# Kernel optimization log

Measured on AMD Instinct MI355X. Metric: run time of the kernel, lower is better.

The kernel has to match this reference:

```python
import jax, jax.numpy as jnp
import numpy as np

B, C, H, W = 16, 64, 128, 128
C8 = C // 8


def setup_inputs() -> dict:
    key = jax.random.key(0)
    ks = jax.random.split(key, 8)
    s = 0.05
    return {
        "x": jax.random.normal(ks[0], (B, C, H, W), dtype=jnp.float32),
        "Wq": jax.random.normal(ks[1], (C8, C), dtype=jnp.float32) * s,
        "bq": jax.random.normal(ks[2], (C8,), dtype=jnp.float32) * s,
        "Wk": jax.random.normal(ks[3], (C8, C), dtype=jnp.float32) * s,
        "bk": jax.random.normal(ks[4], (C8,), dtype=jnp.float32) * s,
        "Wv": jax.random.normal(ks[5], (C, C), dtype=jnp.float32) * s,
        "bv": jax.random.normal(ks[6], (C,), dtype=jnp.float32) * s,
        "gamma": jnp.zeros((1,), dtype=jnp.float32),
    }


def _criss_cross(x, Wq, bq, Wk, bk, Wv, bv, gamma):
    # 1x1 convs == channel-mixing matmuls
    q = jnp.einsum("bchw,oc->bohw", x, Wq) + bq[None, :, None, None]  # [B,C8,H,W]
    k = jnp.einsum("bchw,oc->bohw", x, Wk) + bk[None, :, None, None]  # [B,C8,H,W]
    v = jnp.einsum("bchw,oc->bohw", x, Wv) + bv[None, :, None, None]  # [B,C,H,W]

    h = x.shape[2]
    # column (H-axis) attention scores; diagonal masked to -inf
    energy_H = jnp.einsum("bchw,bciw->bhwi", q, k)  # [B,H,W,H]
    diag = jnp.eye(h, dtype=bool)[None, :, None, :]  # mask where query row == key row
    energy_H = jnp.where(diag, -jnp.inf, energy_H)
    # row (W-axis) attention scores
    energy_W = jnp.einsum("bchw,bchj->bhwj", q, k)  # [B,H,W,W]

    # joint softmax over concatenated H+W axis
    att = jax.nn.softmax(jnp.concatenate([energy_H, energy_W], axis=3), axis=3)
    att_H = att[:, :, :, :h]    # [B,H,W,H]
    att_W = att[:, :, :, h:]    # [B,H,W,W]

    out_H = jnp.einsum("bhwi,bciw->bchw", att_H, v)
    out_W = jnp.einsum("bhwj,bchj->bchw", att_W, v)
    return gamma[0] * (out_H + out_W) + x


def reference(x, Wq, bq, Wk, bk, Wv, bv, gamma):
    return _criss_cross(x, Wq, bq, Wk, bk, Wv, bv, gamma)
```

## Files before the change

### kernel.cpp

```cpp
#include <hip/hip_runtime.h>

#define HW 128
#define CC 64
#define NB 16
#define LOG2E 1.44269504088896f

typedef _Float16 h1;
typedef _Float16 h2 __attribute__((ext_vector_type(2)));
typedef _Float16 half8 __attribute__((ext_vector_type(8)));
typedef float float16v __attribute__((ext_vector_type(16)));
typedef uint uv4 __attribute__((ext_vector_type(4)));

__device__ __forceinline__ uint packh2(float a, float b) {
#if __has_builtin(__builtin_amdgcn_cvt_pkrtz)
  return __builtin_bit_cast(uint, __builtin_amdgcn_cvt_pkrtz(a, b));
#else
  h2 v; v[0] = (h1)a; v[1] = (h1)b; return __builtin_bit_cast(uint, v);
#endif
}
__device__ __forceinline__ ushort f2h(float a) { h1 v = (h1)a; return __builtin_bit_cast(ushort, v); }
__device__ __forceinline__ float  h2f(ushort a) { return (float)__builtin_bit_cast(h1, a); }

__device__ __forceinline__ float fexp2(float x) {
#if __has_builtin(__builtin_amdgcn_exp2f)
  return __builtin_amdgcn_exp2f(x);
#else
  return exp2f(x);
#endif
}

__device__ __forceinline__ float16v mfma16(uv4 a, uv4 b, float16v c) {
  return __builtin_amdgcn_mfma_f32_32x32x16_f16(
      __builtin_bit_cast(half8, a), __builtin_bit_cast(half8, b), c, 0, 0, 0);
}

__global__ __launch_bounds__(256) void k_prep(
    const float* __restrict__ Wq, const float* __restrict__ bq,
    const float* __restrict__ Wk, const float* __restrict__ bk,
    const float* __restrict__ Wv, const float* __restrict__ bv,
    ushort* __restrict__ W_frag, float* __restrict__ bias_f)
{
  int idx = blockIdx.x * 256 + threadIdx.x;
  if (idx < 6144) {
    int g = idx >> 3, e = idx & 7;
    int kshi = g / 96, o = g % 96;
    int ks = kshi >> 1, hi = kshi & 1;
    int c = 8 * hi + 16 * ks + e;
    float val = (o < 8)  ? Wq[o * 64 + c] * LOG2E
              : (o < 16) ? Wk[(o - 8) * 64 + c]
              : (o < 80) ? Wv[(o - 16) * 64 + c] : 0.f;
    W_frag[idx] = f2h(val);
  }
  if (blockIdx.x == 0 && threadIdx.x < 96) {
    int t = threadIdx.x;
    bias_f[t] = (t < 8) ? bq[t] * LOG2E : (t < 16) ? bk[t - 8] : (t < 80) ? bv[t - 16] : 0.f;
  }
}

__global__ __launch_bounds__(256, 4) void k_projW(
    const float* __restrict__ x, const ushort* __restrict__ W_frag,
    const float* __restrict__ bias_f,
    ushort* __restrict__ qT, ushort* __restrict__ kT,
    ushort* __restrict__ v,
    ushort* __restrict__ oW_, float* __restrict__ mW_, float* __restrict__ sW_)
{
  alignas(16) __shared__ uint V_l[64 * 64];
  alignas(16) __shared__ ushort qk_l[128 * 24];
  __shared__ float bias_l[96];

  int t = threadIdx.x;
  int lane = t & 63, wv = t >> 6, hi = lane >> 5;
  int b = blockIdx.x >> 7, r = blockIdx.x & 127;
  if (t < 96) bias_l[t] = bias_f[t];

  int w = 32 * wv + (lane & 31);
  const float* xw = x + (size_t)(b * CC) * (HW * HW) + (size_t)r * HW + w;
  const size_t PL = (size_t)HW * HW;

  float xv[32];
  #pragma unroll
  for (int ks = 0; ks < 4; ++ks) {
    int c0 = 8 * hi + 16 * ks;
    #pragma unroll
    for (int e = 0; e < 8; ++e)
      xv[ks * 8 + e] = xw[(size_t)(c0 + e) * PL];
  }
  __builtin_amdgcn_sched_barrier(0);

  float16v acc0 = {}, acc1 = {}, acc2 = {};
  #pragma unroll
  for (int ks = 0; ks < 4; ++ks) {
    uv4 Bx;
    #pragma unroll
    for (int e2 = 0; e2 < 4; ++e2)
      Bx[e2] = packh2(xv[ks * 8 + 2 * e2], xv[ks * 8 + 2 * e2 + 1]);
    const ushort* wf = W_frag + (size_t)(ks * 2 + hi) * 96 * 8;
    uv4 a0 = *(const uv4*)(wf + (lane & 31) * 8);
    uv4 a1 = *(const uv4*)(wf + ((lane & 31) + 32) * 8);
    uv4 a2 = *(const uv4*)(wf + ((lane & 31) + 64) * 8);
    acc0 = mfma16(a0, Bx, acc0);
    acc1 = mfma16(a1, Bx, acc1);
    acc2 = mfma16(a2, Bx, acc2);
  }
  __syncthreads();

  #pragma unroll
  for (int reg = 0; reg < 16; ++reg) {
    int orow = (reg & 3) + 8 * (reg >> 2) + 4 * hi;
    float v0 = acc0[reg] + bias_l[orow];
    if (orow < 16) {
      qk_l[w * 24 + orow] = f2h(v0);
    } else {
      int c = orow - 16;
      *(ushort*)((char*)V_l + c * 256 + ((2 * w) ^ ((c & 15) << 4))) = f2h(v0);
    }
    int c1 = orow + 16;
    *(ushort*)((char*)V_l + c1 * 256 + ((2 * w) ^ ((c1 & 15) << 4))) =
        f2h(acc1[reg] + bias_l[orow + 32]);
    if (orow < 16) {
      int c2_ = orow + 48;
      *(ushort*)((char*)V_l + c2_ * 256 + ((2 * w) ^ ((c2_ & 15) << 4))) =
          f2h(acc2[reg] + bias_l[orow + 64]);
    }
  }
  __syncthreads();

  ushort* vb = v + (size_t)(b * CC) * PL + (size_t)r * HW;
  #pragma unroll
  for (int i = 0; i < 4; ++i) {
    int idx = t + 256 * i; int c = idx >> 4, j8 = idx & 15;
    uv4 val = *(const uv4*)((const char*)V_l + c * 256 + ((16 * j8) ^ ((c & 15) << 4)));
    *(uv4*)(vb + (size_t)c * PL + j8 * 8) = val;
  }
  {
    int pix = t & 127, isk = t >> 7;
    uv4 val = *(const uv4*)&qk_l[pix * 24 + isk * 8];
    ushort* dstt = (isk ? kT : qT) + ((size_t)(b * HW + pix) * HW + r) * 8;
    *(uv4*)dstt = val;
  }

  int qg = w;
  uv4 Bq = {0, 0, 0, 0};
  uv4 ka[4] = {{0,0,0,0}, {0,0,0,0}, {0,0,0,0}, {0,0,0,0}};
  if (hi == 0) {
    Bq = *(const uv4*)&qk_l[qg * 24];
    #pragma unroll
    for (int mt = 0; mt < 4; ++mt)
      ka[mt] = *(const uv4*)&qk_l[((lane & 31) + 32 * mt) * 24 + 8];
  }

  float16v e[4];
  #pragma unroll
  for (int mt = 0; mt < 4; ++mt) {
    float16v z = {};
    e[mt] = mfma16(ka[mt], Bq, z);
  }

  float m = -INFINITY;
  #pragma unroll
  for (int mt = 0; mt < 4; ++mt)
    #pragma unroll
    for (int reg = 0; reg < 16; reg += 2)
      m = fmaxf(m, fmaxf(e[mt][reg], e[mt][reg + 1]));
  m = fmaxf(m, __shfl_xor(m, 32));

  float s0 = 0.f, s1 = 0.f, s2 = 0.f, s3 = 0.f;
  #pragma unroll
  for (int mt = 0; mt < 4; ++mt) {
    #pragma unroll
    for (int reg = 0; reg < 16; reg += 4) {
      float p0 = fexp2(e[mt][reg + 0] - m);
      float p1 = fexp2(e[mt][reg + 1] - m);
      float p2 = fexp2(e[mt][reg + 2] - m);
      float p3 = fexp2(e[mt][reg + 3] - m);
      e[mt][reg + 0] = p0; e[mt][reg + 1] = p1;
      e[mt][reg + 2] = p2; e[mt][reg + 3] = p3;
      s0 += p0; s1 += p1; s2 += p2; s3 += p3;
    }
  }
  float s = (s0 + s1) + (s2 + s3);
  s += __shfl_xor(s, 32);
  if (lane < 32) {
    mW_[(size_t)blockIdx.x * HW + qg] = m;
    sW_[(size_t)blockIdx.x * HW + qg] = s;
  }

  float16v pacc0 = {}, pacc1 = {};
  #pragma unroll
  for (int s8 = 0; s8 < 8; ++s8) {
    int mt = s8 >> 1, hf = s8 & 1;
    float p0 = e[mt][8 * hf + 0], p1 = e[mt][8 * hf + 1];
    float p2 = e[mt][8 * hf + 2], p3 = e[mt][8 * hf + 3];
    float p4 = e[mt][8 * hf + 4], p5 = e[mt][8 * hf + 5];
    float p6 = e[mt][8 * hf + 6], p7 = e[mt][8 * hf + 7];
    uint X = packh2(p0, p1), Y = packh2(p2, p3), Z = packh2(p4, p5), Wp = packh2(p6, p7);
    uint Xs = __shfl_xor(X, 32), Ys = __shfl_xor(Y, 32);
    uint Zs = __shfl_xor(Z, 32), Ws = __shfl_xor(Wp, 32);
    uv4 Bp;
    Bp[0] = (hi == 0) ? X  : Zs;
    Bp[1] = (hi == 0) ? Y  : Ws;
    Bp[2] = (hi == 0) ? Xs : Z;
    Bp[3] = (hi == 0) ? Ys : Wp;
    #pragma unroll
    for (int ct = 0; ct < 2; ++ct) {
      int c = (lane & 31) + 32 * ct;
      uint byteoff = c * 256 + ((16 * (hi + 2 * s8)) ^ ((c & 15) << 4));
      uv4 va = *(const uv4*)((const char*)V_l + byteoff);
      if (ct == 0) pacc0 = mfma16(va, Bp, pacc0);
      else         pacc1 = mfma16(va, Bp, pacc1);
    }
  }

  __syncthreads();
  ushort* o_l = (ushort*)V_l;
  #pragma unroll
  for (int reg = 0; reg < 16; ++reg) {
    int c = (reg & 3) + 8 * (reg >> 2) + 4 * hi;
    o_l[(c +  0) * 128 + w] = f2h(pacc0[reg]);
    o_l[(c + 32) * 128 + w] = f2h(pacc1[reg]);
  }
  __syncthreads();
  ushort* ob = oW_ + (size_t)(b * CC) * PL + (size_t)r * HW;
  #pragma unroll
  for (int i = 0; i < 4; ++i) {
    int idx = t + 256 * i; int c = idx >> 4, w8 = idx & 15;
    *(uv4*)(ob + (size_t)c * PL + w8 * 8) = *(const uv4*)&o_l[c * 128 + w8 * 8];
  }
}

__global__ __launch_bounds__(256) void k_transpose_v(const ushort* __restrict__ v,
                                                     ushort* __restrict__ vT)
{
  __shared__ ushort tl[128 * 130];
  int t = threadIdx.x;
  size_t base = (size_t)blockIdx.x * (HW * HW);
  const uint* ip = (const uint*)(v + base);
  uint* op = (uint*)(vT + base);
  int c2 = t & 63;
  int r0 = t >> 6;
  for (int it = 0; it < 32; ++it) {
    int r = it * 4 + r0;
    uint val = ip[r * 64 + c2];
    *(uint*)&tl[r * 130 + c2 * 2] = val;
  }
  __syncthreads();
  for (int it = 0; it < 32; ++it) {
    int wcol = it * 4 + r0;
    int hh = c2 * 2;
    uint lo = tl[hh * 130 + wcol];
    uint hi = tl[(hh + 1) * 130 + wcol];
    op[wcol * 64 + c2] = lo | (hi << 16);
  }
}

__global__ __launch_bounds__(256, 4) void k_attnH(
    const ushort* __restrict__ qT, const ushort* __restrict__ kT,
    const ushort* __restrict__ vT,
    const float* __restrict__ mW_, const float* __restrict__ sW_,
    ushort* __restrict__ oH_, ushort* __restrict__ aWn)
{
  alignas(16) __shared__ uint V_l[64 * 64];

  int t = threadIdx.x;
  int lane = t & 63, wv = t >> 6;
  int hi = lane >> 5;
  int bid = blockIdx.x;
  int b = bid >> 7, r = bid & 127;
  size_t plane32 = (size_t)(HW * HW) / 2;
  const size_t PL = (size_t)HW * HW;
  size_t pixbase = (size_t)(b * HW + r) * HW * 8;

  int qg = 32 * wv + (lane & 31);
  uv4 Bq = {0, 0, 0, 0};
  uv4 ka[4] = {{0,0,0,0}, {0,0,0,0}, {0,0,0,0}, {0,0,0,0}};
  if (hi == 0) {
    Bq = *(const uv4*)(qT + pixbase + (size_t)qg * 8);
    #pragma unroll
    for (int mt = 0; mt < 4; ++mt)
      ka[mt] = *(const uv4*)(kT + pixbase + (size_t)((lane & 31) + 32 * mt) * 8);
  }
  float mw = mW_[(size_t)b * PL + (size_t)qg * HW + r];
  float sw = sW_[(size_t)b * PL + (size_t)qg * HW + r];

  const uint* vrow = (const uint*)vT + (size_t)(b * CC) * plane32 + (size_t)r * 64;
  #pragma unroll
  for (int i = 0; i < 4; ++i) {
    int idx = t + 256 * i; int c = idx >> 4, j4 = idx & 15;
    uv4 val = *(const uv4*)(vrow + (size_t)c * plane32 + 4 * j4);
    uint byteoff = c * 256 + ((16 * j4) ^ ((c & 15) << 4));
    *(uv4*)((char*)V_l + byteoff) = val;
  }
  __syncthreads();

  float16v e[4];
  #pragma unroll
  for (int mt = 0; mt < 4; ++mt) {
    float16v z = {};
    e[mt] = mfma16(ka[mt], Bq, z);
  }

  #pragma unroll
  for (int mt = 0; mt < 4; ++mt)
    #pragma unroll
    for (int reg = 0; reg < 16; ++reg) {
      int key = 32 * mt + ((reg & 3) + 8 * (reg >> 2) + 4 * hi);
      e[mt][reg] = (key == qg) ? -INFINITY : e[mt][reg];
    }

  float m = -INFINITY;
  #pragma unroll
  for (int mt = 0; mt < 4; ++mt)
    #pragma unroll
    for (int reg = 0; reg < 16; reg += 2)
      m = fmaxf(m, fmaxf(e[mt][reg], e[mt][reg + 1]));
  m = fmaxf(m, __shfl_xor(m, 32));

  float s0 = 0.f, s1 = 0.f, s2 = 0.f, s3 = 0.f;
  #pragma unroll
  for (int mt = 0; mt < 4; ++mt) {
    #pragma unroll
    for (int reg = 0; reg < 16; reg += 4) {
      float p0 = fexp2(e[mt][reg + 0] - m);
      float p1 = fexp2(e[mt][reg + 1] - m);
      float p2 = fexp2(e[mt][reg + 2] - m);
      float p3 = fexp2(e[mt][reg + 3] - m);
      e[mt][reg + 0] = p0; e[mt][reg + 1] = p1;
      e[mt][reg + 2] = p2; e[mt][reg + 3] = p3;
      s0 += p0; s1 += p1; s2 += p2; s3 += p3;
    }
  }
  float s = (s0 + s1) + (s2 + s3);
  s += __shfl_xor(s, 32);

  float mm = fmaxf(m, mw);
  float eh = fexp2(m - mm), ew = fexp2(mw - mm);
  float inv = 1.f / (s * eh + sw * ew);
  float aH = eh * inv;
  if (hi == 0)
    aWn[(size_t)b * PL + (size_t)qg * HW + r] = f2h(ew * inv);

  float16v acc0 = {}, acc1 = {};
  #pragma unroll
  for (int s8 = 0; s8 < 8; ++s8) {
    int mt = s8 >> 1, hf = s8 & 1;
    float p0 = e[mt][8 * hf + 0], p1 = e[mt][8 * hf + 1];
    float p2 = e[mt][8 * hf + 2], p3 = e[mt][8 * hf + 3];
    float p4 = e[mt][8 * hf + 4], p5 = e[mt][8 * hf + 5];
    float p6 = e[mt][8 * hf + 6], p7 = e[mt][8 * hf + 7];
    uint X = packh2(p0, p1), Y = packh2(p2, p3), Z = packh2(p4, p5), Wp = packh2(p6, p7);
    uint Xs = __shfl_xor(X, 32), Ys = __shfl_xor(Y, 32);
    uint Zs = __shfl_xor(Z, 32), Ws = __shfl_xor(Wp, 32);
    uv4 Bp;
    Bp[0] = (hi == 0) ? X  : Zs;
    Bp[1] = (hi == 0) ? Y  : Ws;
    Bp[2] = (hi == 0) ? Xs : Z;
    Bp[3] = (hi == 0) ? Ys : Wp;
    #pragma unroll
    for (int ct = 0; ct < 2; ++ct) {
      int c = (lane & 31) + 32 * ct;
      uint byteoff = c * 256 + ((16 * (hi + 2 * s8)) ^ ((c & 15) << 4));
      uv4 va = *(const uv4*)((const char*)V_l + byteoff);
      if (ct == 0) acc0 = mfma16(va, Bp, acc0);
      else         acc1 = mfma16(va, Bp, acc1);
    }
  }

  __syncthreads();
  ushort* o_l = (ushort*)V_l;
  int w = 32 * wv + (lane & 31);
  #pragma unroll
  for (int reg = 0; reg < 16; ++reg) {
    int c = (reg & 3) + 8 * (reg >> 2) + 4 * hi;
    o_l[(c +  0) * 128 + w] = f2h(acc0[reg] * aH);
    o_l[(c + 32) * 128 + w] = f2h(acc1[reg] * aH);
  }
  __syncthreads();
  ushort* ob = oH_ + (size_t)(b * CC) * PL + (size_t)r * HW;
  #pragma unroll
  for (int i = 0; i < 4; ++i) {
    int idx = t + 256 * i; int c = idx >> 4, w8 = idx & 15;
    *(uv4*)(ob + (size_t)c * PL + w8 * 8) = *(const uv4*)&o_l[c * 128 + w8 * 8];
  }
}

__global__ __launch_bounds__(256) void k_merge(
    const ushort* __restrict__ oHT, const ushort* __restrict__ oW,
    const ushort* __restrict__ aWn,
    const float* __restrict__ x, const float* __restrict__ gamma,
    float* __restrict__ out)
{
  alignas(16) __shared__ ushort otile[2 * 32 * 132];
  int t = threadIdx.x;
  int bid = blockIdx.x;
  int wsel = bid & 3, cg = (bid >> 2) & 31, b = bid >> 7;
  int w0 = wsel * 32;
  float g = gamma[0];
  const int PL = HW * HW;

  uv4 ov[4];
  #pragma unroll
  for (int i = 0; i < 4; ++i) {
    int p = t + 256 * i;
    int ch = p >> 9, rest = p & 511;
    int w = rest >> 4, hg = rest & 15;
    size_t cbase = (size_t)(b * CC + cg * 2 + ch) * PL;
    ov[i] = *(const uv4*)(oHT + cbase + (size_t)(w0 + w) * HW + hg * 8);
  }
  uint2 owp[8]; float4 xp[8]; uint2 awp[4];
  #pragma unroll
  for (int i = 0; i < 2; ++i) {
    int p = t + 256 * i;
    int w4 = p & 7, hh2 = p >> 3;
    #pragma unroll
    for (int rr = 0; rr < 2; ++rr) {
      int hh = 2 * hh2 + rr;
      size_t poff = (size_t)hh * HW + w0 + 4 * w4;
      awp[i * 2 + rr] = *(const uint2*)(aWn + (size_t)b * PL + poff);
      #pragma unroll
      for (int ch = 0; ch < 2; ++ch) {
        size_t base = (size_t)(b * CC + cg * 2 + ch) * PL + poff;
        owp[ch * 4 + i * 2 + rr] = *(const uint2*)(oW + base);
        xp[ch * 4 + i * 2 + rr]  = *(const float4*)(x + base);
      }
    }
  }
  #pragma unroll
  for (int i = 0; i < 4; ++i) {
    int p = t + 256 * i;
    int ch = p >> 9, rest = p & 511;
    int w = rest >> 4, hg = rest & 15;
    *(uv4*)&otile[(ch * 32 + w) * 132 + hg * 8] = ov[i];
  }
  __syncthreads();

  #pragma unroll
  for (int ch = 0; ch < 2; ++ch) {
    size_t cbase = (size_t)(b * CC + cg * 2 + ch) * PL;
    const ushort* otc = &otile[ch * 32 * 132];
    #pragma unroll
    for (int i = 0; i < 2; ++i) {
      int p = t + 256 * i;
      int w4 = p & 7, hh2 = p >> 3;
      float th0[4], th1[4];
      #pragma unroll
      for (int j = 0; j < 4; ++j) {
        uint pk = *(const uint*)&otc[(4 * w4 + j) * 132 + 2 * hh2];
        th0[j] = h2f((ushort)(pk & 0xffff));
        th1[j] = h2f((ushort)(pk >> 16));
      }
      #pragma unroll
      for (int rr = 0; rr < 2; ++rr) {
        int hh = 2 * hh2 + rr;
        const float* th = rr ? th1 : th0;
        size_t base = cbase + (size_t)hh * HW + w0 + 4 * w4;
        uint2 aw2 = awp[i * 2 + rr];
        uint2 ow2 = owp[ch * 4 + i * 2 + rr];
        float4 xv = xp[ch * 4 + i * 2 + rr];
        float4 res;
        res.x = g * (th[0] + h2f((ushort)(ow2.x & 0xffff)) * h2f((ushort)(aw2.x & 0xffff))) + xv.x;
        res.y = g * (th[1] + h2f((ushort)(ow2.x >> 16))    * h2f((ushort)(aw2.x >> 16)))    + xv.y;
        res.z = g * (th[2] + h2f((ushort)(ow2.y & 0xffff)) * h2f((ushort)(aw2.y & 0xffff))) + xv.z;
        res.w = g * (th[3] + h2f((ushort)(ow2.y >> 16))    * h2f((ushort)(aw2.y >> 16)))    + xv.w;
        *(float4*)(out + base) = res;
      }
    }
  }
}

extern "C" void kernel_launch(void* const* d_in, const int* in_sizes, int n_in,
                              void* d_out, int out_size, void* d_ws, size_t ws_size,
                              hipStream_t stream)
{
  const float* x     = (const float*)d_in[0];
  const float* Wq    = (const float*)d_in[1];
  const float* bq    = (const float*)d_in[2];
  const float* Wk    = (const float*)d_in[3];
  const float* bk    = (const float*)d_in[4];
  const float* Wv    = (const float*)d_in[5];
  const float* bv    = (const float*)d_in[6];
  const float* gamma = (const float*)d_in[7];
  float* out = (float*)d_out;

  char* w = (char*)d_ws;
  size_t np = (size_t)NB * HW * HW;
  ushort* W_frag = (ushort*)w; w += 6144 * 2;
  float*  bias_f = (float*)w;  w += 96 * 4 + 320;
  ushort* qT  = (ushort*)w;  w += np * 8 * 2;
  ushort* kT  = (ushort*)w;  w += np * 8 * 2;
  ushort* v   = (ushort*)w;  w += np * CC * 2;
  ushort* vT  = (ushort*)w;  w += np * CC * 2;
  ushort* oW  = (ushort*)w;  w += np * CC * 2;
  ushort* oHT = (ushort*)w;  w += np * CC * 2;
  float* mW = (float*)w;  w += np * 4;
  float* sW = (float*)w;  w += np * 4;
  ushort* aWn = (ushort*)w; w += np * 2;
  if ((size_t)(w - (char*)d_ws) > ws_size) return;

  k_prep<<<24, 256, 0, stream>>>(Wq, bq, Wk, bk, Wv, bv, W_frag, bias_f);
  k_projW<<<NB * HW, 256, 0, stream>>>(x, W_frag, bias_f, qT, kT, v, oW, mW, sW);
  k_transpose_v<<<NB * CC, 256, 0, stream>>>(v, vT);
  k_attnH<<<NB * HW, 256, 0, stream>>>(qT, kT, vT, mW, sW, oHT, aWn);
  k_merge<<<NB * 32 * 4, 256, 0, stream>>>(oHT, oW, aWn, x, gamma, out);
}
```

Measured before the change: 103.3 us.

## Fuse V transpose into projection kernel and drop separate transpose pass

The projection kernel now writes V directly in transposed layout (element-wise 2-byte scattered stores at stride HW), which removes the separate k_transpose_v kernel and the intermediate v buffer round trip. Loads of x are interleaved with packing instead of being prefetched into 32 registers, and launch bounds are raised to 6 waves per SIMD for occupancy. The scattered 2-byte stores are poorly coalesced (each row block writes one element per 256-byte line), which may cost more write bandwidth than the removed kernel saved.

Result: slower. 210.7 us (+104.0%).

```diff
diff --git a/kernel.cpp b/kernel.cpp
--- a/kernel.cpp
+++ b/kernel.cpp
@@ -57,11 +57,11 @@
   }
 }
 
-__global__ __launch_bounds__(256, 4) void k_projW(
+__global__ __launch_bounds__(256, 6) void k_projW(
     const float* __restrict__ x, const ushort* __restrict__ W_frag,
     const float* __restrict__ bias_f,
     ushort* __restrict__ qT, ushort* __restrict__ kT,
-    ushort* __restrict__ v,
+    ushort* __restrict__ vT,
     ushort* __restrict__ oW_, float* __restrict__ mW_, float* __restrict__ sW_)
 {
   alignas(16) __shared__ uint V_l[64 * 64];
@@ -77,23 +77,18 @@
   const float* xw = x + (size_t)(b * CC) * (HW * HW) + (size_t)r * HW + w;
   const size_t PL = (size_t)HW * HW;
 
-  float xv[32];
+  float16v acc0 = {}, acc1 = {}, acc2 = {};
   #pragma unroll
   for (int ks = 0; ks < 4; ++ks) {
     int c0 = 8 * hi + 16 * ks;
-    #pragma unroll
-    for (int e = 0; e < 8; ++e)
-      xv[ks * 8 + e] = xw[(size_t)(c0 + e) * PL];
-  }
-  __builtin_amdgcn_sched_barrier(0);
-
-  float16v acc0 = {}, acc1 = {}, acc2 = {};
-  #pragma unroll
-  for (int ks = 0; ks < 4; ++ks) {
-    uv4 Bx;
-    #pragma unroll
-    for (int e2 = 0; e2 < 4; ++e2)
-      Bx[e2] = packh2(xv[ks * 8 + 2 * e2], xv[ks * 8 + 2 * e2 + 1]);
+    uint bx[4];
+    #pragma unroll
+    for (int e2 = 0; e2 < 4; ++e2) {
+      float f0 = xw[(size_t)(c0 + 2 * e2) * PL];
+      float f1 = xw[(size_t)(c0 + 2 * e2 + 1) * PL];
+      bx[e2] = packh2(f0, f1);
+    }
+    uv4 Bx = {bx[0], bx[1], bx[2], bx[3]};
     const ushort* wf = W_frag + (size_t)(ks * 2 + hi) * 96 * 8;
     uv4 a0 = *(const uv4*)(wf + (lane & 31) * 8);
     uv4 a1 = *(const uv4*)(wf + ((lane & 31) + 32) * 8);
@@ -125,12 +120,14 @@
   }
   __syncthreads();
 
-  ushort* vb = v + (size_t)(b * CC) * PL + (size_t)r * HW;
-  #pragma unroll
-  for (int i = 0; i < 4; ++i) {
-    int idx = t + 256 * i; int c = idx >> 4, j8 = idx & 15;
-    uv4 val = *(const uv4*)((const char*)V_l + c * 256 + ((16 * j8) ^ ((c & 15) << 4)));
-    *(uv4*)(vb + (size_t)c * PL + j8 * 8) = val;
+  {
+    ushort* vtb = vT + (size_t)(b * CC) * PL + r;
+    #pragma unroll
+    for (int i = 0; i < 32; ++i) {
+      int idx = t + 256 * i; int c = idx >> 7, ww = idx & 127;
+      ushort val = *(const ushort*)((const char*)V_l + c * 256 + ((2 * ww) ^ ((c & 15) << 4)));
+      vtb[(size_t)c * PL + (size_t)ww * HW] = val;
+    }
   }
   {
     int pix = t & 127, isk = t >> 7;
@@ -225,31 +222,6 @@
   for (int i = 0; i < 4; ++i) {
     int idx = t + 256 * i; int c = idx >> 4, w8 = idx & 15;
     *(uv4*)(ob + (size_t)c * PL + w8 * 8) = *(const uv4*)&o_l[c * 128 + w8 * 8];
-  }
-}
-
-__global__ __launch_bounds__(256) void k_transpose_v(const ushort* __restrict__ v,
-                                                     ushort* __restrict__ vT)
-{
-  __shared__ ushort tl[128 * 130];
-  int t = threadIdx.x;
-  size_t base = (size_t)blockIdx.x * (HW * HW);
-  const uint* ip = (const uint*)(v + base);
-  uint* op = (uint*)(vT + base);
-  int c2 = t & 63;
-  int r0 = t >> 6;
-  for (int it = 0; it < 32; ++it) {
-    int r = it * 4 + r0;
-    uint val = ip[r * 64 + c2];
-    *(uint*)&tl[r * 130 + c2 * 2] = val;
-  }
-  __syncthreads();
-  for (int it = 0; it < 32; ++it) {
-    int wcol = it * 4 + r0;
-    int hh = c2 * 2;
-    uint lo = tl[hh * 130 + wcol];
-    uint hi = tl[(hh + 1) * 130 + wcol];
-    op[wcol * 64 + c2] = lo | (hi << 16);
   }
 }
 
@@ -487,7 +459,6 @@
   float*  bias_f = (float*)w;  w += 96 * 4 + 320;
   ushort* qT  = (ushort*)w;  w += np * 8 * 2;
   ushort* kT  = (ushort*)w;  w += np * 8 * 2;
-  ushort* v   = (ushort*)w;  w += np * CC * 2;
   ushort* vT  = (ushort*)w;  w += np * CC * 2;
   ushort* oW  = (ushort*)w;  w += np * CC * 2;
   ushort* oHT = (ushort*)w;  w += np * CC * 2;
@@ -497,8 +468,7 @@
   if ((size_t)(w - (char*)d_ws) > ws_size) return;
 
   k_prep<<<24, 256, 0, stream>>>(Wq, bq, Wk, bk, Wv, bv, W_frag, bias_f);
-  k_projW<<<NB * HW, 256, 0, stream>>>(x, W_frag, bias_f, qT, kT, v, oW, mW, sW);
-  k_transpose_v<<<NB * CC, 256, 0, stream>>>(v, vT);
+  k_projW<<<NB * HW, 256, 0, stream>>>(x, W_frag, bias_f, qT, kT, vT, oW, mW, sW);
   k_attnH<<<NB * HW, 256, 0, stream>>>(qT, kT, vT, mW, sW, oHT, aWn);
   k_merge<<<NB * 32 * 4, 256, 0, stream>>>(oHT, oW, aWn, x, gamma, out);
 }
```
